# Optimization experiments

Measured on AMD Instinct MI355X. Metric: run time of the kernel, lower is better.

Reference implementation:

```python
import jax
import jax.numpy as jnp
import numpy as np
from jax import lax

B, L, H, M = 32768, 128, 256, 16


def setup_inputs() -> dict:
    key = jax.random.key(0)
    ks = jax.random.split(key, 7)
    s_ih = 1.0 / np.sqrt(H)  # PyTorch GRUCell init scale (uniform bound); use scaled normal
    return {
        "x": jax.random.randint(ks[0], (B, L), 0, M, dtype=jnp.int32),
        "W_ih": jax.random.normal(ks[1], (3 * H, 1), dtype=jnp.float32) * s_ih,
        "W_hh": jax.random.normal(ks[2], (3 * H, H), dtype=jnp.float32) * s_ih,
        "b_ih": jax.random.normal(ks[3], (3 * H,), dtype=jnp.float32) * s_ih,
        "b_hh": jax.random.normal(ks[4], (3 * H,), dtype=jnp.float32) * s_ih,
        "W_fc": jax.random.normal(ks[5], (M, H), dtype=jnp.float32) * s_ih,
        "b_fc": jax.random.normal(ks[6], (M,), dtype=jnp.float32) * s_ih,
    }


def reference(x, W_ih, W_hh, b_ih, b_hh, W_fc, b_fc):
    # (zeros at i=0) as a scalar feature; output log_softmax gathered at x[:, i].
    xf = x.astype(jnp.float32)
    x_in = jnp.concatenate([jnp.zeros((x.shape[0], 1), jnp.float32), xf[:, :-1]], axis=1)  # [B, L]

    def step(h, inp):
        x_t, tgt = inp  # x_t: [B] float, tgt: [B] int
        gi = x_t[:, None] * W_ih.T + b_ih            # [B, 3H] (input dim is 1)
        gh = h @ W_hh.T + b_hh                       # [B, 3H]
        ir, iz, i_n = jnp.split(gi, 3, axis=1)
        hr, hz, h_n = jnp.split(gh, 3, axis=1)
        r = jax.nn.sigmoid(ir + hr)
        z = jax.nn.sigmoid(iz + hz)
        n = jnp.tanh(i_n + r * h_n)
        h_new = (1.0 - z) * n + z * h                # [B, H]
        logp = jax.nn.log_softmax(h_new @ W_fc.T + b_fc, axis=1)  # [B, M]
        lp = jnp.take_along_axis(logp, tgt[:, None], axis=1)[:, 0]  # [B]
        return h_new, lp

    h0 = jnp.zeros((x.shape[0], W_hh.shape[1]), jnp.float32)
    _, lps = lax.scan(step, h0, (x_in.T, x.T))  # lps: [L, B]
    return lps.sum(axis=0)  # [B] log_probsum
```

## Files before the change

### kernel.cpp

```cpp
#include <hip/hip_runtime.h>

typedef __attribute__((ext_vector_type(8))) short s16x8;
typedef __attribute__((ext_vector_type(4))) float f32x4;
typedef __attribute__((ext_vector_type(16))) float f32x16;

#define BATCH 32768
#define LSEQ 128
#define W32_SHORTS (8 * 4 * 17 * 512)
#define WFC_SHORTS 4096
#define XT_OFF_BYTES ((W32_SHORTS + WFC_SHORTS) * 2)
#define WS_NEED_XT (XT_OFF_BYTES + BATCH * LSEQ * 4)

#define HROW 264
#define HBUF_S (128 * HROW)
#define LDS_BYTES (2 * HBUF_S * 2)

#define L2E 1.4426950408889634f
#define LN2 0.6931471805599453f

#define MFMA32(A, B, C) __builtin_amdgcn_mfma_f32_32x32x16_bf16(A, B, C, 0, 0, 0)

__device__ __forceinline__ unsigned short f2b(float f) {
  unsigned u = __float_as_uint(f);
  u += 0x7FFFu + ((u >> 16) & 1u);
  return (unsigned short)(u >> 16);
}

__device__ __forceinline__ float exp2n(float x) { float r; asm("v_exp_f32 %0, -%1" : "=v"(r) : "v"(x)); return r; }
__device__ __forceinline__ float exp2p(float x) { float r; asm("v_exp_f32 %0, %1" : "=v"(r) : "v"(x)); return r; }
__device__ __forceinline__ float rcp_(float x)  { float r; asm("v_rcp_f32 %0, %1" : "=v"(r) : "v"(x)); return r; }
__device__ __forceinline__ float log2_(float x) { float r; asm("v_log_f32 %0, %1" : "=v"(r) : "v"(x)); return r; }
__device__ __forceinline__ unsigned cvtpk(float lo, float hi) {
  unsigned r; asm("v_cvt_pk_bf16_f32 %0, %1, %2" : "=v"(r) : "v"(lo), "v"(hi)); return r;
}

__global__ void gru_prep(const float* __restrict__ Wih, const float* __restrict__ Whh,
                         const float* __restrict__ bih, const float* __restrict__ bhh,
                         const float* __restrict__ Wfc,
                         unsigned short* __restrict__ wfrag,
                         unsigned short* __restrict__ wfc16) {
  int t = blockIdx.x * 256 + threadIdx.x;
  if (t < W32_SHORTS) {
    int e = t & 7, lane = (t >> 3) & 63, frag = t >> 9;
    int ks = frag % 17, g = (frag / 17) & 3, tr = frag / 68;
    int l31 = lane & 31, hh = lane >> 5;
    int k = (ks < 16) ? ks * 16 + hh * 8 + e : 256 + hh * 8 + e;
    float val = 0.f;
    if (g < 3) {
      int j = g * 256 + tr * 32 + l31;
      if (k < 256) val = Whh[j * 256 + k];
      else if (k == 256) val = (g < 2) ? Wih[j] : 0.f;
      else if (k == 257) val = (g < 2) ? (bih[j] + bhh[j]) : bhh[j];
    } else if (ks == 16) {
      int j = 512 + tr * 32 + l31;
      if (k == 256) val = Wih[j];
      else if (k == 257) val = bih[j];
    }
    wfrag[t] = f2b(val);
  } else if (t < W32_SHORTS + WFC_SHORTS) {
    int t2 = t - W32_SHORTS;
    wfc16[t2] = f2b(Wfc[t2]);
  }
}

__global__ void x_transpose(const int* __restrict__ x, int* __restrict__ xT) {
  __shared__ int tile[32][33];
  int l0 = blockIdx.x * 32, b0 = blockIdx.y * 32;
  for (int r = threadIdx.y; r < 32; r += 8)
    tile[r][threadIdx.x] = x[(b0 + r) * LSEQ + l0 + threadIdx.x];
  __syncthreads();
  for (int r = threadIdx.y; r < 32; r += 8)
    xT[(l0 + r) * BATCH + b0 + threadIdx.x] = tile[threadIdx.x][r];
}

template <int XT>
__global__ __attribute__((amdgpu_waves_per_eu(2, 2))) __launch_bounds__(512)
void gru_main(const int* __restrict__ x, const int* __restrict__ xTr,
              const unsigned short* __restrict__ wfrag,
              const unsigned short* __restrict__ wfc16,
              const float* __restrict__ bfc, float* __restrict__ out) {
  extern __shared__ unsigned short sm[];

  const int tid = threadIdx.x;
  const int lane = tid & 63;
  const int wv = tid >> 6;
  const int tr = wv;
  const int l31 = lane & 31;
  const int hh = lane >> 5;
  const int q = lane >> 4;
  const int b = lane & 15;
  const int bbase = blockIdx.x * 128;

  {
    unsigned int* p = (unsigned int*)sm;
    for (int r = tid; r < HBUF_S / 2; r += 512) p[r] = 0u;
  }

  float bfc4[4];
#pragma unroll
  for (int r = 0; r < 4; ++r) bfc4[r] = bfc[q * 4 + r];

  const int offR = ((tr * 4 + 0) * 17) * 512 + lane * 8;
  const int offZ = ((tr * 4 + 1) * 17) * 512 + lane * 8;
  const int offH = ((tr * 4 + 2) * 17) * 512 + lane * 8;
  const int offI = ((tr * 4 + 3) * 17) * 512 + lane * 8;
  const int offFC = b * 256 + q * 8;

  const f32x16 z16 = {0, 0, 0, 0, 0, 0, 0, 0, 0, 0, 0, 0, 0, 0, 0, 0};

  float lp = 0.f;
  __syncthreads();

#pragma unroll 1
  for (int i = 0; i < LSEQ; ++i) {
    const unsigned short* rdb = sm + (i & 1) * HBUF_S;
    unsigned short* wrb = sm + ((i & 1) ^ 1) * HBUF_S;

    unsigned long wfu = (unsigned long)wfrag;
    asm volatile("" : "+s"(wfu));
    const unsigned short* wfp = (const unsigned short*)wfu;
    const unsigned short* fR = wfp + offR;
    const unsigned short* fZ = wfp + offZ;
    const unsigned short* fH = wfp + offH;
    const unsigned short* fI = wfp + offI;
    unsigned long wcu = (unsigned long)wfc16;
    asm volatile("" : "+s"(wcu));
    const unsigned short* fFC = (const unsigned short*)wcu + offFC;

#pragma unroll
    for (int p = 0; p < 2; ++p) {
      const int b0 = 2 * p, b1 = 2 * p + 1;

      float xv0, xv1;
      if (XT) {
        xv0 = (i > 0) ? (float)xTr[(i - 1) * BATCH + bbase + b0 * 32 + l31] : 0.f;
        xv1 = (i > 0) ? (float)xTr[(i - 1) * BATCH + bbase + b1 * 32 + l31] : 0.f;
      } else {
        xv0 = (i > 0) ? (float)x[(bbase + b0 * 32 + l31) * LSEQ + i - 1] : 0.f;
        xv1 = (i > 0) ? (float)x[(bbase + b1 * 32 + l31) * LSEQ + i - 1] : 0.f;
      }
      union { unsigned u[4]; s16x8 v; } xf0, xf1;
      xf0.u[0] = (hh == 0) ? ((__float_as_uint(xv0) >> 16) | 0x3F800000u) : 0u;
      xf0.u[1] = xf0.u[2] = xf0.u[3] = 0u;
      xf1.u[0] = (hh == 0) ? ((__float_as_uint(xv1) >> 16) | 0x3F800000u) : 0u;
      xf1.u[1] = xf1.u[2] = xf1.u[3] = 0u;

      s16x8 gR = *(const s16x8*)(fR + 16 * 512);
      s16x8 gZ = *(const s16x8*)(fZ + 16 * 512);
      s16x8 gH = *(const s16x8*)(fH + 16 * 512);
      s16x8 gI = *(const s16x8*)(fI + 16 * 512);
      f32x16 R0 = MFMA32(gR, xf0.v, z16), R1 = MFMA32(gR, xf1.v, z16);
      f32x16 Z0 = MFMA32(gZ, xf0.v, z16), Z1 = MFMA32(gZ, xf1.v, z16);
      f32x16 H0 = MFMA32(gH, xf0.v, z16), H1 = MFMA32(gH, xf1.v, z16);
      f32x16 I0 = MFMA32(gI, xf0.v, z16), I1 = MFMA32(gI, xf1.v, z16);

      s16x8 c0r = *(const s16x8*)(fR + 0 * 512);
      s16x8 c0z = *(const s16x8*)(fZ + 0 * 512);
      s16x8 c0h = *(const s16x8*)(fH + 0 * 512);
      s16x8 c1r = *(const s16x8*)(fR + 1 * 512);
      s16x8 c1z = *(const s16x8*)(fZ + 1 * 512);
      s16x8 c1h = *(const s16x8*)(fH + 1 * 512);

      const unsigned short* r0b = rdb + (b0 * 32 + l31) * HROW;
      const unsigned short* r1b = rdb + (b1 * 32 + l31) * HROW;

#pragma unroll
      for (int it = 0; it < 8; ++it) {
        s16x8 n0r, n0z, n0h, n1r, n1z, n1h;
        if (it < 7) {
          n0r = *(const s16x8*)(fR + (2 * it + 2) * 512);
          n0z = *(const s16x8*)(fZ + (2 * it + 2) * 512);
          n0h = *(const s16x8*)(fH + (2 * it + 2) * 512);
          n1r = *(const s16x8*)(fR + (2 * it + 3) * 512);
          n1z = *(const s16x8*)(fZ + (2 * it + 3) * 512);
          n1h = *(const s16x8*)(fH + (2 * it + 3) * 512);
        }
        {
          const s16x8 hA = *(const s16x8*)&r0b[16 * (2 * it) + 8 * hh];
          const s16x8 hB = *(const s16x8*)&r1b[16 * (2 * it) + 8 * hh];
          R0 = MFMA32(c0r, hA, R0); Z0 = MFMA32(c0z, hA, Z0); H0 = MFMA32(c0h, hA, H0);
          R1 = MFMA32(c0r, hB, R1); Z1 = MFMA32(c0z, hB, Z1); H1 = MFMA32(c0h, hB, H1);
        }
        {
          const s16x8 hA = *(const s16x8*)&r0b[16 * (2 * it + 1) + 8 * hh];
          const s16x8 hB = *(const s16x8*)&r1b[16 * (2 * it + 1) + 8 * hh];
          R0 = MFMA32(c1r, hA, R0); Z0 = MFMA32(c1z, hA, Z0); H0 = MFMA32(c1h, hA, H0);
          R1 = MFMA32(c1r, hB, R1); Z1 = MFMA32(c1z, hB, Z1); H1 = MFMA32(c1h, hB, H1);
        }
        if (it < 7) { c0r = n0r; c0z = n0z; c0h = n0h; c1r = n1r; c1z = n1z; c1h = n1h; }
      }

      auto epilogue = [&](int bg, const f32x16& R, const f32x16& Zg,
                          const f32x16& Hg, const f32x16& Ig) {
        const int hrow = bg * 32 + l31;
        const unsigned short* hpb = rdb + hrow * HROW;
        unsigned short* hwb = wrb + hrow * HROW;
#pragma unroll
        for (int rq = 0; rq < 4; ++rq) {
          const int col = tr * 32 + 4 * hh + 8 * rq;
          const uint2 hp = *(const uint2*)&hpb[col];
          const float hpv[4] = {
              __uint_as_float(hp.x << 16), __uint_as_float(hp.x & 0xFFFF0000u),
              __uint_as_float(hp.y << 16), __uint_as_float(hp.y & 0xFFFF0000u)};
          float hv[4];
#pragma unroll
          for (int e2 = 0; e2 < 4; ++e2) {
            const int idx = rq * 4 + e2;
            float rr = rcp_(1.f + exp2n(L2E * R[idx]));
            float zz = rcp_(1.f + exp2n(L2E * Zg[idx]));
            float y  = fmaf(rr, Hg[idx], Ig[idx]);
            float u  = rcp_(1.f + exp2p((2.f * L2E) * y));
            float nn = fmaf(-2.f, u, 1.f);
            hv[e2] = fmaf(zz, hpv[e2] - nn, nn);
          }
          *(uint2*)&hwb[col] = make_uint2(cvtpk(hv[0], hv[1]), cvtpk(hv[2], hv[3]));
        }
      };
      epilogue(b0, R0, Z0, H0, I0);
      epilogue(b1, R1, Z1, H1, I1);
    }

    __syncthreads();

    {
      const int lrow = wv * 16 + b;
      const int grow = bbase + lrow;
      f32x4 fa = {bfc4[0], bfc4[1], bfc4[2], bfc4[3]};
      const unsigned short* hbb = wrb + lrow * HROW;
#pragma unroll
      for (int ks = 0; ks < 8; ++ks) {
        s16x8 wf = *(const s16x8*)(fFC + 32 * ks);
        s16x8 hb = *(const s16x8*)&hbb[32 * ks + 8 * q];
        fa = __builtin_amdgcn_mfma_f32_16x16x32_bf16(wf, hb, fa, 0, 0, 0);
      }
      int tgt = XT ? xTr[i * BATCH + grow] : x[grow * LSEQ + i];
      float l0 = fa[0], l1 = fa[1], l2 = fa[2], l3 = fa[3];
      float mx = fmaxf(fmaxf(l0, l1), fmaxf(l2, l3));
      mx = fmaxf(mx, __shfl_xor(mx, 16));
      mx = fmaxf(mx, __shfl_xor(mx, 32));
      float se = exp2p(L2E * (l0 - mx)) + exp2p(L2E * (l1 - mx)) +
                 exp2p(L2E * (l2 - mx)) + exp2p(L2E * (l3 - mx));
      se += __shfl_xor(se, 16);
      se += __shfl_xor(se, 32);
      float v01 = (tgt & 1) ? l1 : l0;
      float v23 = (tgt & 1) ? l3 : l2;
      float vs = (tgt & 2) ? v23 : v01;
      float contrib = (q == (tgt >> 2)) ? vs : 0.f;
      contrib += __shfl_xor(contrib, 16);
      contrib += __shfl_xor(contrib, 32);
      lp += contrib - mx - LN2 * log2_(se);
    }
  }

  if (q == 0) out[bbase + wv * 16 + b] = lp;
}

extern "C" void kernel_launch(void* const* d_in, const int* in_sizes, int n_in,
                              void* d_out, int out_size, void* d_ws, size_t ws_size,
                              hipStream_t stream) {
  (void)in_sizes; (void)n_in; (void)out_size;
  const int*   x   = (const int*)d_in[0];
  const float* Wih = (const float*)d_in[1];
  const float* Whh = (const float*)d_in[2];
  const float* bih = (const float*)d_in[3];
  const float* bhh = (const float*)d_in[4];
  const float* Wfc = (const float*)d_in[5];
  const float* bfc = (const float*)d_in[6];
  float* out = (float*)d_out;

  unsigned short* wfrag = (unsigned short*)d_ws;
  unsigned short* wfc16 = wfrag + W32_SHORTS;
  int* xT = (int*)((char*)d_ws + XT_OFF_BYTES);

  gru_prep<<<dim3((W32_SHORTS + WFC_SHORTS) / 256), dim3(256), 0, stream>>>(
      Wih, Whh, bih, bhh, Wfc, wfrag, wfc16);

  if (ws_size >= (size_t)WS_NEED_XT) {
    x_transpose<<<dim3(LSEQ / 32, BATCH / 32), dim3(32, 8), 0, stream>>>(x, xT);
    hipFuncSetAttribute((const void*)gru_main<1>,
                        hipFuncAttributeMaxDynamicSharedMemorySize, LDS_BYTES);
    gru_main<1><<<dim3(256), dim3(512), LDS_BYTES, stream>>>(x, xT, wfrag, wfc16, bfc, out);
  } else {
    hipFuncSetAttribute((const void*)gru_main<0>,
                        hipFuncAttributeMaxDynamicSharedMemorySize, LDS_BYTES);
    gru_main<0><<<dim3(256), dim3(512), LDS_BYTES, stream>>>(x, x, wfrag, wfc16, bfc, out);
  }
}
```

Before: 2.042 ms.

## Process all four batch groups per K-step and compute input gate on VALU

Restructures the GRU recurrent matmul loop to handle all four 32-row batch groups in one K loop, so each weight fragment is loaded once per step rather than twice. The n-gate input term is no longer produced by an MFMA; it is computed in the epilogue from per-lane packed bf16 W_ih/b_ih registers with an FMA. Together these cut global weight loads and MFMA count per step, at the cost of many more live accumulators (12 f32x16), which raises register pressure at the fixed 2 waves/EU.

```diff
diff --git a/kernel.cpp b/kernel.cpp
--- a/kernel.cpp
+++ b/kernel.cpp
@@ -19,6 +19,7 @@
 #define LN2 0.6931471805599453f
 
 #define MFMA32(A, B, C) __builtin_amdgcn_mfma_f32_32x32x16_bf16(A, B, C, 0, 0, 0)
+#define MFMA16(A, B, C) __builtin_amdgcn_mfma_f32_16x16x32_bf16(A, B, C, 0, 0, 0)
 
 __device__ __forceinline__ unsigned short f2b(float f) {
   unsigned u = __float_as_uint(f);
@@ -51,10 +52,6 @@
       if (k < 256) val = Whh[j * 256 + k];
       else if (k == 256) val = (g < 2) ? Wih[j] : 0.f;
       else if (k == 257) val = (g < 2) ? (bih[j] + bhh[j]) : bhh[j];
-    } else if (ks == 16) {
-      int j = 512 + tr * 32 + l31;
-      if (k == 256) val = Wih[j];
-      else if (k == 257) val = bih[j];
     }
     wfrag[t] = f2b(val);
   } else if (t < W32_SHORTS + WFC_SHORTS) {
@@ -78,8 +75,11 @@
 void gru_main(const int* __restrict__ x, const int* __restrict__ xTr,
               const unsigned short* __restrict__ wfrag,
               const unsigned short* __restrict__ wfc16,
+              const float* __restrict__ Wih, const float* __restrict__ bih,
               const float* __restrict__ bfc, float* __restrict__ out) {
   extern __shared__ unsigned short sm[];
+  unsigned short* h0 = sm;
+  unsigned short* h1 = sm + HBUF_S;
 
   const int tid = threadIdx.x;
   const int lane = tid & 63;
@@ -92,19 +92,21 @@
   const int bbase = blockIdx.x * 128;
 
   {
-    unsigned int* p = (unsigned int*)sm;
-    for (int r = tid; r < HBUF_S / 2; r += 512) p[r] = 0u;
-  }
-
+    unsigned int* p = (unsigned int*)h0;
+#pragma unroll
+    for (int r = 0; r < 33; ++r) p[tid + r * 512] = 0u;
+  }
+
+  unsigned winbin[16];
+#pragma unroll
+  for (int reg = 0; reg < 16; ++reg) {
+    int crow = (reg & 3) + 8 * (reg >> 2) + 4 * hh;
+    int j = 512 + tr * 32 + crow;
+    winbin[reg] = (unsigned)f2b(Wih[j]) | ((unsigned)f2b(bih[j]) << 16);
+  }
   float bfc4[4];
 #pragma unroll
   for (int r = 0; r < 4; ++r) bfc4[r] = bfc[q * 4 + r];
-
-  const int offR = ((tr * 4 + 0) * 17) * 512 + lane * 8;
-  const int offZ = ((tr * 4 + 1) * 17) * 512 + lane * 8;
-  const int offH = ((tr * 4 + 2) * 17) * 512 + lane * 8;
-  const int offI = ((tr * 4 + 3) * 17) * 512 + lane * 8;
-  const int offFC = b * 256 + q * 8;
 
   const f32x16 z16 = {0, 0, 0, 0, 0, 0, 0, 0, 0, 0, 0, 0, 0, 0, 0, 0};
 
@@ -113,111 +115,97 @@
 
 #pragma unroll 1
   for (int i = 0; i < LSEQ; ++i) {
-    const unsigned short* rdb = sm + (i & 1) * HBUF_S;
-    unsigned short* wrb = sm + ((i & 1) ^ 1) * HBUF_S;
+    const unsigned short* rdb = (i & 1) ? h1 : h0;
+    unsigned short* wrb = (i & 1) ? h0 : h1;
 
     unsigned long wfu = (unsigned long)wfrag;
     asm volatile("" : "+s"(wfu));
     const unsigned short* wfp = (const unsigned short*)wfu;
-    const unsigned short* fR = wfp + offR;
-    const unsigned short* fZ = wfp + offZ;
-    const unsigned short* fH = wfp + offH;
-    const unsigned short* fI = wfp + offI;
     unsigned long wcu = (unsigned long)wfc16;
     asm volatile("" : "+s"(wcu));
-    const unsigned short* fFC = (const unsigned short*)wcu + offFC;
-
-#pragma unroll
-    for (int p = 0; p < 2; ++p) {
-      const int b0 = 2 * p, b1 = 2 * p + 1;
-
-      float xv0, xv1;
-      if (XT) {
-        xv0 = (i > 0) ? (float)xTr[(i - 1) * BATCH + bbase + b0 * 32 + l31] : 0.f;
-        xv1 = (i > 0) ? (float)xTr[(i - 1) * BATCH + bbase + b1 * 32 + l31] : 0.f;
-      } else {
-        xv0 = (i > 0) ? (float)x[(bbase + b0 * 32 + l31) * LSEQ + i - 1] : 0.f;
-        xv1 = (i > 0) ? (float)x[(bbase + b1 * 32 + l31) * LSEQ + i - 1] : 0.f;
-      }
-      union { unsigned u[4]; s16x8 v; } xf0, xf1;
-      xf0.u[0] = (hh == 0) ? ((__float_as_uint(xv0) >> 16) | 0x3F800000u) : 0u;
-      xf0.u[1] = xf0.u[2] = xf0.u[3] = 0u;
-      xf1.u[0] = (hh == 0) ? ((__float_as_uint(xv1) >> 16) | 0x3F800000u) : 0u;
-      xf1.u[1] = xf1.u[2] = xf1.u[3] = 0u;
-
-      s16x8 gR = *(const s16x8*)(fR + 16 * 512);
-      s16x8 gZ = *(const s16x8*)(fZ + 16 * 512);
-      s16x8 gH = *(const s16x8*)(fH + 16 * 512);
-      s16x8 gI = *(const s16x8*)(fI + 16 * 512);
-      f32x16 R0 = MFMA32(gR, xf0.v, z16), R1 = MFMA32(gR, xf1.v, z16);
-      f32x16 Z0 = MFMA32(gZ, xf0.v, z16), Z1 = MFMA32(gZ, xf1.v, z16);
-      f32x16 H0 = MFMA32(gH, xf0.v, z16), H1 = MFMA32(gH, xf1.v, z16);
-      f32x16 I0 = MFMA32(gI, xf0.v, z16), I1 = MFMA32(gI, xf1.v, z16);
-
-      s16x8 c0r = *(const s16x8*)(fR + 0 * 512);
-      s16x8 c0z = *(const s16x8*)(fZ + 0 * 512);
-      s16x8 c0h = *(const s16x8*)(fH + 0 * 512);
-      s16x8 c1r = *(const s16x8*)(fR + 1 * 512);
-      s16x8 c1z = *(const s16x8*)(fZ + 1 * 512);
-      s16x8 c1h = *(const s16x8*)(fH + 1 * 512);
-
-      const unsigned short* r0b = rdb + (b0 * 32 + l31) * HROW;
-      const unsigned short* r1b = rdb + (b1 * 32 + l31) * HROW;
-
-#pragma unroll
-      for (int it = 0; it < 8; ++it) {
-        s16x8 n0r, n0z, n0h, n1r, n1z, n1h;
-        if (it < 7) {
-          n0r = *(const s16x8*)(fR + (2 * it + 2) * 512);
-          n0z = *(const s16x8*)(fZ + (2 * it + 2) * 512);
-          n0h = *(const s16x8*)(fH + (2 * it + 2) * 512);
-          n1r = *(const s16x8*)(fR + (2 * it + 3) * 512);
-          n1z = *(const s16x8*)(fZ + (2 * it + 3) * 512);
-          n1h = *(const s16x8*)(fH + (2 * it + 3) * 512);
+    const unsigned short* wc = (const unsigned short*)wcu;
+
+    const unsigned short* fR = wfp + ((tr * 4 + 0) * 17) * 512 + lane * 8;
+    const unsigned short* fZ = wfp + ((tr * 4 + 1) * 17) * 512 + lane * 8;
+    const unsigned short* fH = wfp + ((tr * 4 + 2) * 17) * 512 + lane * 8;
+
+    float xin4[4];
+    unsigned xlo[4];
+#pragma unroll
+    for (int bg = 0; bg < 4; ++bg) {
+      float xv;
+      if (XT) xv = (i > 0) ? (float)xTr[(i - 1) * BATCH + bbase + bg * 32 + l31] : 0.f;
+      else    xv = (i > 0) ? (float)x[(bbase + bg * 32 + l31) * LSEQ + i - 1] : 0.f;
+      xin4[bg] = xv;
+      xlo[bg] = (hh == 0) ? ((__float_as_uint(xv) >> 16) | 0x3F800000u) : 0u;
+    }
+
+    s16x8 ar = *(const s16x8*)(fR + 16 * 512);
+    s16x8 az = *(const s16x8*)(fZ + 16 * 512);
+    s16x8 ah = *(const s16x8*)(fH + 16 * 512);
+    f32x16 aRc[4], aZc[4], aHc[4];
+#pragma unroll
+    for (int bg = 0; bg < 4; ++bg) {
+      union { unsigned u[4]; s16x8 v; } xf;
+      xf.u[0] = xlo[bg]; xf.u[1] = xf.u[2] = xf.u[3] = 0u;
+      aRc[bg] = MFMA32(ar, xf.v, z16);
+      aZc[bg] = MFMA32(az, xf.v, z16);
+      aHc[bg] = MFMA32(ah, xf.v, z16);
+    }
+
+    const unsigned short* rb[4];
+#pragma unroll
+    for (int bg = 0; bg < 4; ++bg) rb[bg] = rdb + (bg * 32 + l31) * HROW + 8 * hh;
+
+    s16x8 cr = *(const s16x8*)(fR);
+    s16x8 cz = *(const s16x8*)(fZ);
+    s16x8 ch = *(const s16x8*)(fH);
+#pragma unroll
+    for (int ks = 0; ks < 16; ++ks) {
+      s16x8 nr, nz, nh;
+      if (ks < 15) {
+        nr = *(const s16x8*)(fR + (ks + 1) * 512);
+        nz = *(const s16x8*)(fZ + (ks + 1) * 512);
+        nh = *(const s16x8*)(fH + (ks + 1) * 512);
+      }
+#pragma unroll
+      for (int bg = 0; bg < 4; ++bg) {
+        const s16x8 hb = *(const s16x8*)&rb[bg][ks * 16];
+        aRc[bg] = MFMA32(cr, hb, aRc[bg]);
+        aZc[bg] = MFMA32(cz, hb, aZc[bg]);
+        aHc[bg] = MFMA32(ch, hb, aHc[bg]);
+      }
+      if (ks < 15) { cr = nr; cz = nz; ch = nh; }
+    }
+
+#pragma unroll
+    for (int bg = 0; bg < 4; ++bg) {
+      const float xv = xin4[bg];
+      const int rowb = (bg * 32 + l31) * HROW;
+#pragma unroll
+      for (int rq = 0; rq < 4; ++rq) {
+        const int col = tr * 32 + 4 * hh + 8 * rq;
+        const uint2 hp = *(const uint2*)&rdb[rowb + col];
+        const float hpv[4] = {
+            __uint_as_float(hp.x << 16), __uint_as_float(hp.x & 0xFFFF0000u),
+            __uint_as_float(hp.y << 16), __uint_as_float(hp.y & 0xFFFF0000u)};
+        float hv[4];
+#pragma unroll
+        for (int e2 = 0; e2 < 4; ++e2) {
+          const int idx = rq * 4 + e2;
+          const unsigned u = winbin[idx];
+          const float inr = fmaf(xv, __uint_as_float(u << 16),
+                                 __uint_as_float(u & 0xFFFF0000u));
+          float rr = rcp_(1.f + exp2n(L2E * aRc[bg][idx]));
+          float zz = rcp_(1.f + exp2n(L2E * aZc[bg][idx]));
+          float y  = fmaf(rr, aHc[bg][idx], inr);
+          float uu = rcp_(1.f + exp2p((2.f * L2E) * y));
+          float nn = fmaf(-2.f, uu, 1.f);
+          hv[e2] = fmaf(zz, hpv[e2] - nn, nn);
         }
-        {
-          const s16x8 hA = *(const s16x8*)&r0b[16 * (2 * it) + 8 * hh];
-          const s16x8 hB = *(const s16x8*)&r1b[16 * (2 * it) + 8 * hh];
-          R0 = MFMA32(c0r, hA, R0); Z0 = MFMA32(c0z, hA, Z0); H0 = MFMA32(c0h, hA, H0);
-          R1 = MFMA32(c0r, hB, R1); Z1 = MFMA32(c0z, hB, Z1); H1 = MFMA32(c0h, hB, H1);
-        }
-        {
-          const s16x8 hA = *(const s16x8*)&r0b[16 * (2 * it + 1) + 8 * hh];
-          const s16x8 hB = *(const s16x8*)&r1b[16 * (2 * it + 1) + 8 * hh];
-          R0 = MFMA32(c1r, hA, R0); Z0 = MFMA32(c1z, hA, Z0); H0 = MFMA32(c1h, hA, H0);
-          R1 = MFMA32(c1r, hB, R1); Z1 = MFMA32(c1z, hB, Z1); H1 = MFMA32(c1h, hB, H1);
-        }
-        if (it < 7) { c0r = n0r; c0z = n0z; c0h = n0h; c1r = n1r; c1z = n1z; c1h = n1h; }
-      }
-
-      auto epilogue = [&](int bg, const f32x16& R, const f32x16& Zg,
-                          const f32x16& Hg, const f32x16& Ig) {
-        const int hrow = bg * 32 + l31;
-        const unsigned short* hpb = rdb + hrow * HROW;
-        unsigned short* hwb = wrb + hrow * HROW;
-#pragma unroll
-        for (int rq = 0; rq < 4; ++rq) {
-          const int col = tr * 32 + 4 * hh + 8 * rq;
-          const uint2 hp = *(const uint2*)&hpb[col];
-          const float hpv[4] = {
-              __uint_as_float(hp.x << 16), __uint_as_float(hp.x & 0xFFFF0000u),
-              __uint_as_float(hp.y << 16), __uint_as_float(hp.y & 0xFFFF0000u)};
-          float hv[4];
-#pragma unroll
-          for (int e2 = 0; e2 < 4; ++e2) {
-            const int idx = rq * 4 + e2;
-            float rr = rcp_(1.f + exp2n(L2E * R[idx]));
-            float zz = rcp_(1.f + exp2n(L2E * Zg[idx]));
-            float y  = fmaf(rr, Hg[idx], Ig[idx]);
-            float u  = rcp_(1.f + exp2p((2.f * L2E) * y));
-            float nn = fmaf(-2.f, u, 1.f);
-            hv[e2] = fmaf(zz, hpv[e2] - nn, nn);
-          }
-          *(uint2*)&hwb[col] = make_uint2(cvtpk(hv[0], hv[1]), cvtpk(hv[2], hv[3]));
-        }
-      };
-      epilogue(b0, R0, Z0, H0, I0);
-      epilogue(b1, R1, Z1, H1, I1);
+        *(uint2*)&wrb[rowb + col] =
+            make_uint2(cvtpk(hv[0], hv[1]), cvtpk(hv[2], hv[3]));
+      }
     }
 
     __syncthreads();
@@ -226,12 +214,13 @@
       const int lrow = wv * 16 + b;
       const int grow = bbase + lrow;
       f32x4 fa = {bfc4[0], bfc4[1], bfc4[2], bfc4[3]};
-      const unsigned short* hbb = wrb + lrow * HROW;
+      const unsigned short* hbb = wrb + lrow * HROW + 8 * q;
+      const unsigned short* wcb = wc + b * 256 + q * 8;
 #pragma unroll
       for (int ks = 0; ks < 8; ++ks) {
-        s16x8 wf = *(const s16x8*)(fFC + 32 * ks);
-        s16x8 hb = *(const s16x8*)&hbb[32 * ks + 8 * q];
-        fa = __builtin_amdgcn_mfma_f32_16x16x32_bf16(wf, hb, fa, 0, 0, 0);
+        s16x8 wfcf = *(const s16x8*)(wcb + 32 * ks);
+        s16x8 hb = *(const s16x8*)(hbb + 32 * ks);
+        fa = MFMA16(wfcf, hb, fa);
       }
       int tgt = XT ? xTr[i * BATCH + grow] : x[grow * LSEQ + i];
       float l0 = fa[0], l1 = fa[1], l2 = fa[2], l3 = fa[3];
@@ -279,10 +268,12 @@
     x_transpose<<<dim3(LSEQ / 32, BATCH / 32), dim3(32, 8), 0, stream>>>(x, xT);
     hipFuncSetAttribute((const void*)gru_main<1>,
                         hipFuncAttributeMaxDynamicSharedMemorySize, LDS_BYTES);
-    gru_main<1><<<dim3(256), dim3(512), LDS_BYTES, stream>>>(x, xT, wfrag, wfc16, bfc, out);
+    gru_main<1><<<dim3(256), dim3(512), LDS_BYTES, stream>>>(x, xT, wfrag, wfc16,
+                                                             Wih, bih, bfc, out);
   } else {
     hipFuncSetAttribute((const void*)gru_main<0>,
                         hipFuncAttributeMaxDynamicSharedMemorySize, LDS_BYTES);
-    gru_main<0><<<dim3(256), dim3(512), LDS_BYTES, stream>>>(x, x, wfrag, wfc16, bfc, out);
-  }
-}
+    gru_main<0><<<dim3(256), dim3(512), LDS_BYTES, stream>>>(x, x, wfrag, wfc16,
+                                                             Wih, bih, bfc, out);
+  }
+}
```

Result: slower. 3.898 ms (+90.8%).
